# Kernel optimization log

Measured on AMD Instinct MI355X. Metric: run time of the kernel, lower is better.

Reference implementation:

```python
import jax, jax.numpy as jnp
import numpy as np

B, T, E, H = 4, 2048, 1024, 16
S = E // H  # 64


def setup_inputs() -> dict:
    key = jax.random.key(0)
    ks = jax.random.split(key, 6)
    return {
        "x": jax.random.normal(ks[0], (B, T, E), dtype=jnp.float32),
        "Wk": jax.random.normal(ks[1], (S, S), dtype=jnp.float32) * (1.0 / np.sqrt(S)),
        "Wq": jax.random.normal(ks[2], (S, S), dtype=jnp.float32) * (1.0 / np.sqrt(S)),
        "Wv": jax.random.normal(ks[3], (S, S), dtype=jnp.float32) * (1.0 / np.sqrt(S)),
        "Wp": jax.random.normal(ks[4], (E, E), dtype=jnp.float32) * (1.0 / np.sqrt(E)),
        "bp": jnp.zeros((E,), dtype=jnp.float32),
    }


def reference(x, Wk, Wq, Wv, Wp, bp):
    b, t, e = x.shape
    h, s = H, S
    xh = x.reshape(b, t, h, s)
    # per-head projections share one (s,s) weight across all heads (torch Linear: y = x @ W.T)
    keys = jnp.einsum('bthi,oi->bhto', xh, Wk)     # (b,h,t,s)
    queries = jnp.einsum('bthi,oi->bhto', xh, Wq)
    values = jnp.einsum('bthi,oi->bhto', xh, Wv)
    scale = e ** 0.25  # q and k each divided by e^(1/4) -> net 1/sqrt(e)
    queries = queries / scale
    keys = keys / scale
    dot = jnp.einsum('bhqs,bhks->bhqk', queries, keys)  # (b,h,t,t)
    attn = jax.nn.softmax(dot, axis=-1)
    out = jnp.einsum('bhqk,bhks->bqhs', attn, values)   # (b,t,h,s)
    out = out.reshape(b, t, h * s)
    return jnp.einsum('bte,oe->bto', out, Wp) + bp
```

## Files before the change

kernel.cpp:

```cpp
#include <hip/hip_runtime.h>
#include <hip/hip_bf16.h>

#define Bv 4
#define Tv 2048
#define Ev 1024
#define Hv 16
#define Sv 64

typedef __attribute__((ext_vector_type(8))) short bf16x8;
typedef __attribute__((ext_vector_type(4))) short bf16x4;
typedef __attribute__((ext_vector_type(4))) float f32x4;
typedef __attribute__((ext_vector_type(16))) float f32x16;

__device__ __forceinline__ ushort f2bf(float f) {
    unsigned u = __float_as_uint(f);
    u = (u + 0x7FFFu + ((u >> 16) & 1u)) >> 16;
    return (ushort)u;
}
__device__ __forceinline__ unsigned pkrn(float a, float b) {
    __hip_bfloat162 t = __float22bfloat162_rn(make_float2(a, b));
    unsigned r; __builtin_memcpy(&r, &t, 4); return r;
}
__device__ __forceinline__ unsigned pktr(float a, float b) {
    return __builtin_amdgcn_perm(__float_as_uint(b), __float_as_uint(a), 0x07060302u);
}

__device__ __forceinline__ void async16(void* lds, const void* g) {
    __builtin_amdgcn_global_load_lds(
        (const __attribute__((address_space(1))) unsigned int*)g,
        (__attribute__((address_space(3))) unsigned int*)lds, 16, 0, 0);
}

__global__ __launch_bounds__(256) void cast_kernel(
    const float* __restrict__ Wp, const float* __restrict__ Wq,
    const float* __restrict__ Wk, const float* __restrict__ Wv,
    ushort* __restrict__ Wpb, ushort* __restrict__ Wqb,
    ushort* __restrict__ Wkb, ushort* __restrict__ Wvb)
{
    int blk = blockIdx.x;
    if (blk < 1024) {
        int i = (blk * 256 + threadIdx.x) * 4;
        float4 v = *(const float4*)(Wp + i);
        uint2 o = {pkrn(v.x, v.y), pkrn(v.z, v.w)};
        *(uint2*)(Wpb + i) = o;
    } else {
        int p = blk - 1024;
        const float* src = (p == 0) ? Wq : ((p == 1) ? Wk : Wv);
        ushort* dst      = (p == 0) ? Wqb : ((p == 1) ? Wkb : Wvb);
        const float scale = (p == 0) ? 0.03125f * 1.4426950408889634f : 1.0f;
        #pragma unroll
        for (int it = 0; it < 4; ++it) {
            int i = (it * 256 + threadIdx.x) * 4;
            float4 v = *(const float4*)(src + i);
            uint2 o = {pkrn(v.x * scale, v.y * scale), pkrn(v.z * scale, v.w * scale)};
            *(uint2*)(dst + i) = o;
        }
    }
}

__global__ __launch_bounds__(192) void qkv_kernel(
    const float* __restrict__ x,
    const ushort* __restrict__ Wqb, const ushort* __restrict__ Wkb,
    const ushort* __restrict__ Wvb,
    ushort* __restrict__ Q, ushort* __restrict__ K, ushort* __restrict__ Vt)
{
    const int tid  = threadIdx.x;
    const int wave = tid >> 6;
    const int lane = tid & 63;
    const int m    = lane & 15;
    const int quad = lane >> 4;

    const ushort* Wsel = (wave == 0) ? Wqb : ((wave == 1) ? Wkb : Wvb);
    bf16x8 wf[4][2];
    #pragma unroll
    for (int ot = 0; ot < 4; ++ot)
        #pragma unroll
        for (int ks = 0; ks < 2; ++ks)
            wf[ot][ks] = *(const bf16x8*)&Wsel[(ot * 16 + m) * 64 + ks * 32 + quad * 8];

    const int tt = blockIdx.x >> 2;
    const int hg = blockIdx.x & 3;
    const int g0 = tt * 16;
    const int gm = g0 + m;
    const int b  = g0 >> 11;
    const int t0 = g0 & 2047;

    #pragma unroll
    for (int hi = 0; hi < 4; ++hi) {
        const int h  = hg * 4 + hi;
        const int bh = b * Hv + h;

        bf16x8 xf[2];
        #pragma unroll
        for (int ks = 0; ks < 2; ++ks) {
            const float* src = x + (size_t)gm * Ev + h * Sv + ks * 32 + quad * 8;
            float4 v0 = *(const float4*)src;
            float4 v1 = *(const float4*)(src + 4);
            unsigned pk[4];
            pk[0] = pkrn(v0.x, v0.y); pk[1] = pkrn(v0.z, v0.w);
            pk[2] = pkrn(v1.x, v1.y); pk[3] = pkrn(v1.z, v1.w);
            xf[ks] = *(bf16x8*)pk;
        }

        f32x4 acc[4];
        #pragma unroll
        for (int ot = 0; ot < 4; ++ot) acc[ot] = (f32x4){0.f, 0.f, 0.f, 0.f};

        if (wave < 2) {
            #pragma unroll
            for (int ks = 0; ks < 2; ++ks)
                #pragma unroll
                for (int ot = 0; ot < 4; ++ot)
                    acc[ot] = __builtin_amdgcn_mfma_f32_16x16x32_bf16(
                        wf[ot][ks], xf[ks], acc[ot], 0, 0, 0);
            ushort* dst = ((wave == 0) ? Q : K)
                        + ((size_t)bh * Tv + t0 + m) * Sv + quad * 4;
            #pragma unroll
            for (int ot = 0; ot < 4; ++ot) {
                uint2 w = {pkrn(acc[ot][0], acc[ot][1]), pkrn(acc[ot][2], acc[ot][3])};
                *(uint2*)(dst + ot * 16) = w;
            }
        } else {
            #pragma unroll
            for (int ks = 0; ks < 2; ++ks)
                #pragma unroll
                for (int st = 0; st < 4; ++st)
                    acc[st] = __builtin_amdgcn_mfma_f32_16x16x32_bf16(
                        xf[ks], wf[st][ks], acc[st], 0, 0, 0);
            ushort* vr = Vt + ((size_t)bh * Sv + m) * Tv + t0 + quad * 4;
            #pragma unroll
            for (int st = 0; st < 4; ++st) {
                uint2 w = {pkrn(acc[st][0], acc[st][1]), pkrn(acc[st][2], acc[st][3])};
                *(uint2*)(vr + (size_t)st * 16 * Tv) = w;
            }
        }
    }
}

__global__ __launch_bounds__(256, 4) void attn_kernel(
    const ushort* __restrict__ Q, const ushort* __restrict__ K,
    const ushort* __restrict__ Vt, ushort* __restrict__ O)
{
    __shared__ ushort kl[64 * 64];
    __shared__ ushort vl[64 * 64];
    __shared__ float  ll[4][32];

    const int tid  = threadIdx.x;
    const int wave = tid >> 6;
    const int lane = tid & 63;
    const int r31  = lane & 31;
    const int hi   = lane >> 5;
    const int bh   = blockIdx.x & 63;
    const int q0   = (blockIdx.x >> 6) << 7;

    const ushort* Qb = Q + ((size_t)bh * Tv + q0 + wave * 32 + r31) * Sv + hi * 8;
    bf16x8 qf[4];
    #pragma unroll
    for (int ks = 0; ks < 4; ++ks)
        qf[ks] = *(const bf16x8*)(Qb + ks * 16);

    f32x16 oa[2];
    #pragma unroll
    for (int st = 0; st < 2; ++st)
        #pragma unroll
        for (int r = 0; r < 16; ++r)
            oa[st][r] = 0.f;
    float lsum = 0.f;

    const ushort* Kb = K  + (size_t)bh * Tv * Sv;
    const ushort* Vb = Vt + (size_t)bh * Sv * Tv;

    const int r0 = tid >> 3,         cg0 = (tid & 7) ^ (r0 & 7);
    const int r1 = (256 + tid) >> 3, cg1 = ((256 + tid) & 7) ^ (r1 & 7);
    const size_t koff0 = (size_t)r0 * Sv + cg0 * 8;
    const size_t koff1 = (size_t)r1 * Sv + cg1 * 8;
    const size_t voff0 = (size_t)r0 * Tv + cg0 * 8;
    const size_t voff1 = (size_t)r1 * Tv + cg1 * 8;
    const int swz = r31 & 7;

    for (int k0 = 0; k0 < Tv; k0 += 64) {
        __syncthreads();
        async16(&kl[(size_t)tid * 8],         Kb + (size_t)k0 * Sv + koff0);
        async16(&kl[((size_t)tid + 256) * 8], Kb + (size_t)k0 * Sv + koff1);
        async16(&vl[(size_t)tid * 8],         Vb + k0 + voff0);
        async16(&vl[((size_t)tid + 256) * 8], Vb + k0 + voff1);
        __syncthreads();

        #pragma unroll
        for (int kt = 0; kt < 2; ++kt) {
            f32x16 sacc;
            #pragma unroll
            for (int r = 0; r < 16; ++r) sacc[r] = 0.f;
            #pragma unroll
            for (int ks = 0; ks < 4; ++ks) {
                bf16x8 kf = *(const bf16x8*)
                    &kl[(kt * 32 + r31) * 64 + (((ks * 2 + hi) ^ swz) * 8)];
                sacc = __builtin_amdgcn_mfma_f32_32x32x16_bf16(
                    kf, qf[ks], sacc, 0, 0, 0);
            }

            #pragma unroll
            for (int kp = 0; kp < 2; ++kp) {
                float p[8];
                #pragma unroll
                for (int j = 0; j < 8; ++j)
                    p[j] = __builtin_amdgcn_exp2f(sacc[kp * 8 + j]);
                lsum += ((p[0] + p[1]) + (p[2] + p[3]))
                      + ((p[4] + p[5]) + (p[6] + p[7]));
                unsigned d0 = pktr(p[0], p[1]);
                unsigned d1 = pktr(p[2], p[3]);
                unsigned d2 = pktr(p[4], p[5]);
                unsigned d3 = pktr(p[6], p[7]);
                asm volatile("v_permlane32_swap_b32 %0, %1"
                             : "+v"(d0), "+v"(d2));
                asm volatile("v_permlane32_swap_b32 %0, %1"
                             : "+v"(d1), "+v"(d3));
                unsigned pw[4] = {d0, d1, d2, d3};
                bf16x8 pf = *(bf16x8*)pw;

                const int kc = (kt * 2 + kp) * 2 + hi;
                #pragma unroll
                for (int st = 0; st < 2; ++st) {
                    bf16x8 vf = *(const bf16x8*)
                        &vl[(st * 32 + r31) * 64 + ((kc ^ swz) * 8)];
                    oa[st] = __builtin_amdgcn_mfma_f32_32x32x16_bf16(
                        pf, vf, oa[st], 0, 0, 0);
                }
            }
        }
    }

    lsum += __shfl_xor(lsum, 32, 64);
    if (lane < 32) ll[wave][lane] = 1.0f / lsum;

    float sc[16];
    #pragma unroll
    for (int r = 0; r < 16; ++r)
        sc[r] = ll[wave][(r & 3) + 4 * hi + 8 * (r >> 2)];

    const int b = bh >> 4, h = bh & 15;
    #pragma unroll
    for (int st = 0; st < 2; ++st)
        #pragma unroll
        for (int r = 0; r < 16; ++r) {
            const int q = (r & 3) + 4 * hi + 8 * (r >> 2);
            O[((size_t)(b * Tv + q0 + wave * 32 + q)) * Ev
              + h * Sv + st * 32 + r31] = f2bf(oa[st][r] * sc[r]);
        }
}

__global__ __launch_bounds__(256) void proj_kernel(
    const ushort* __restrict__ A, const ushort* __restrict__ B,
    const float* __restrict__ bp, float* __restrict__ C)
{
    __shared__ ushort Asm[128 * 32];
    __shared__ ushort Bsm[128 * 32];
    const int tid  = threadIdx.x;
    const int wave = tid >> 6;
    const int lane = tid & 63;
    const int m    = lane & 15;
    const int quad = lane >> 4;
    const int wm   = wave >> 1;
    const int wn   = wave & 1;
    const int m0   = blockIdx.x * 128;
    const int n0   = blockIdx.y * 128;

    f32x4 acc[4][4];
    #pragma unroll
    for (int i = 0; i < 4; ++i)
        #pragma unroll
        for (int j = 0; j < 4; ++j)
            acc[i][j] = (f32x4){0.f, 0.f, 0.f, 0.f};

    for (int k0 = 0; k0 < Ev; k0 += 32) {
        __syncthreads();
        #pragma unroll
        for (int j = 0; j < 2; ++j) {
            int c   = j * 256 + tid;
            int row = c >> 2;
            int col = (c & 3) * 8;
            async16(&Asm[c * 8], &A[(size_t)(m0 + row) * Ev + k0 + col]);
            async16(&Bsm[c * 8], &B[(size_t)(n0 + row) * Ev + k0 + col]);
        }
        __syncthreads();

        bf16x8 af[4], bf[4];
        #pragma unroll
        for (int i = 0; i < 4; ++i)
            af[i] = *(const bf16x8*)&Asm[(wm * 64 + i * 16 + m) * 32 + quad * 8];
        #pragma unroll
        for (int j = 0; j < 4; ++j)
            bf[j] = *(const bf16x8*)&Bsm[(wn * 64 + j * 16 + m) * 32 + quad * 8];
        #pragma unroll
        for (int i = 0; i < 4; ++i)
            #pragma unroll
            for (int j = 0; j < 4; ++j)
                acc[i][j] = __builtin_amdgcn_mfma_f32_16x16x32_bf16(
                    af[i], bf[j], acc[i][j], 0, 0, 0);
    }

    float bbv[4];
    #pragma unroll
    for (int j = 0; j < 4; ++j)
        bbv[j] = bp[n0 + wn * 64 + j * 16 + m];

    #pragma unroll
    for (int i = 0; i < 4; ++i)
        #pragma unroll
        for (int j = 0; j < 4; ++j)
            #pragma unroll
            for (int r = 0; r < 4; ++r)
                C[(size_t)(m0 + wm * 64 + i * 16 + quad * 4 + r) * Ev
                  + n0 + wn * 64 + j * 16 + m] = acc[i][j][r] + bbv[j];
}

extern "C" void kernel_launch(void* const* d_in, const int* in_sizes, int n_in,
                              void* d_out, int out_size, void* d_ws, size_t ws_size,
                              hipStream_t stream) {
    const float* x  = (const float*)d_in[0];
    const float* Wk = (const float*)d_in[1];
    const float* Wq = (const float*)d_in[2];
    const float* Wv = (const float*)d_in[3];
    const float* Wp = (const float*)d_in[4];
    const float* bp = (const float*)d_in[5];
    float* out = (float*)d_out;

    ushort* Q   = (ushort*)d_ws;
    ushort* K   = Q   + 8388608;
    ushort* Vt  = K   + 8388608;
    ushort* O   = Vt  + 8388608;
    ushort* Wpb = O   + 8388608;
    ushort* Wqb = Wpb + 1048576;
    ushort* Wkb = Wqb + 4096;
    ushort* Wvb = Wkb + 4096;

    cast_kernel<<<1027, 256, 0, stream>>>(Wp, Wq, Wk, Wv, Wpb, Wqb, Wkb, Wvb);
    qkv_kernel<<<2048, 192, 0, stream>>>(x, Wqb, Wkb, Wvb, Q, K, Vt);
    attn_kernel<<<1024, 256, 0, stream>>>(Q, K, Vt, O);
    proj_kernel<<<dim3(64, 8), 256, 0, stream>>>(O, Wpb, bp, out);
}
```

Measured before the change: 222.2 us.

## Process two 32-query groups per wave in attention to reuse K/V fragments

```diff
diff --git a/kernel.cpp b/kernel.cpp
--- a/kernel.cpp
+++ b/kernel.cpp
@@ -137,13 +137,13 @@
     }
 }
 
-__global__ __launch_bounds__(256, 4) void attn_kernel(
+__global__ __launch_bounds__(256, 2) void attn_kernel(
     const ushort* __restrict__ Q, const ushort* __restrict__ K,
     const ushort* __restrict__ Vt, ushort* __restrict__ O)
 {
     __shared__ ushort kl[64 * 64];
     __shared__ ushort vl[64 * 64];
-    __shared__ float  ll[4][32];
+    __shared__ float  ll[4][64];
 
     const int tid  = threadIdx.x;
     const int wave = tid >> 6;
@@ -151,21 +151,25 @@
     const int r31  = lane & 31;
     const int hi   = lane >> 5;
     const int bh   = blockIdx.x & 63;
-    const int q0   = (blockIdx.x >> 6) << 7;
-
-    const ushort* Qb = Q + ((size_t)bh * Tv + q0 + wave * 32 + r31) * Sv + hi * 8;
-    bf16x8 qf[4];
-    #pragma unroll
-    for (int ks = 0; ks < 4; ++ks)
-        qf[ks] = *(const bf16x8*)(Qb + ks * 16);
-
-    f32x16 oa[2];
-    #pragma unroll
-    for (int st = 0; st < 2; ++st)
-        #pragma unroll
-        for (int r = 0; r < 16; ++r)
-            oa[st][r] = 0.f;
-    float lsum = 0.f;
+    const int q0   = (blockIdx.x >> 6) << 8;
+
+    const ushort* Qb = Q + ((size_t)bh * Tv + q0 + wave * 64 + r31) * Sv + hi * 8;
+    bf16x8 qf[2][4];
+    #pragma unroll
+    for (int g = 0; g < 2; ++g)
+        #pragma unroll
+        for (int ks = 0; ks < 4; ++ks)
+            qf[g][ks] = *(const bf16x8*)(Qb + (size_t)g * 32 * Sv + ks * 16);
+
+    f32x16 oa[2][2];
+    #pragma unroll
+    for (int g = 0; g < 2; ++g)
+        #pragma unroll
+        for (int st = 0; st < 2; ++st)
+            #pragma unroll
+            for (int r = 0; r < 16; ++r)
+                oa[g][st][r] = 0.f;
+    float lsum[2] = {0.f, 0.f};
 
     const ushort* Kb = K  + (size_t)bh * Tv * Sv;
     const ushort* Vb = Vt + (size_t)bh * Sv * Tv;
@@ -178,6 +182,28 @@
     const size_t voff1 = (size_t)r1 * Tv + cg1 * 8;
     const int swz = r31 & 7;
 
+    auto softpv = [&](const f32x16& sv, float& ls, f32x16* oag, int kp,
+                      const bf16x8* vf) {
+        float p[8];
+        #pragma unroll
+        for (int j = 0; j < 8; ++j)
+            p[j] = __builtin_amdgcn_exp2f(sv[kp * 8 + j]);
+        ls += ((p[0] + p[1]) + (p[2] + p[3]))
+            + ((p[4] + p[5]) + (p[6] + p[7]));
+        unsigned d0 = pktr(p[0], p[1]);
+        unsigned d1 = pktr(p[2], p[3]);
+        unsigned d2 = pktr(p[4], p[5]);
+        unsigned d3 = pktr(p[6], p[7]);
+        asm volatile("v_permlane32_swap_b32 %0, %1" : "+v"(d0), "+v"(d2));
+        asm volatile("v_permlane32_swap_b32 %0, %1" : "+v"(d1), "+v"(d3));
+        unsigned pw[4] = {d0, d1, d2, d3};
+        bf16x8 pf = *(bf16x8*)pw;
+        #pragma unroll
+        for (int st = 0; st < 2; ++st)
+            oag[st] = __builtin_amdgcn_mfma_f32_32x32x16_bf16(
+                pf, vf[st], oag[st], 0, 0, 0);
+    };
+
     for (int k0 = 0; k0 < Tv; k0 += 64) {
         __syncthreads();
         async16(&kl[(size_t)tid * 8],         Kb + (size_t)k0 * Sv + koff0);
@@ -188,65 +214,61 @@
 
         #pragma unroll
         for (int kt = 0; kt < 2; ++kt) {
-            f32x16 sacc;
-            #pragma unroll
-            for (int r = 0; r < 16; ++r) sacc[r] = 0.f;
-            #pragma unroll
-            for (int ks = 0; ks < 4; ++ks) {
-                bf16x8 kf = *(const bf16x8*)
+            bf16x8 kf[4];
+            #pragma unroll
+            for (int ks = 0; ks < 4; ++ks)
+                kf[ks] = *(const bf16x8*)
                     &kl[(kt * 32 + r31) * 64 + (((ks * 2 + hi) ^ swz) * 8)];
-                sacc = __builtin_amdgcn_mfma_f32_32x32x16_bf16(
-                    kf, qf[ks], sacc, 0, 0, 0);
+
+            f32x16 s0, s1;
+            #pragma unroll
+            for (int r = 0; r < 16; ++r) { s0[r] = 0.f; s1[r] = 0.f; }
+            #pragma unroll
+            for (int ks = 0; ks < 4; ++ks)
+                s0 = __builtin_amdgcn_mfma_f32_32x32x16_bf16(
+                    kf[ks], qf[0][ks], s0, 0, 0, 0);
+            #pragma unroll
+            for (int ks = 0; ks < 4; ++ks)
+                s1 = __builtin_amdgcn_mfma_f32_32x32x16_bf16(
+                    kf[ks], qf[1][ks], s1, 0, 0, 0);
+
+            #pragma unroll
+            for (int kp = 0; kp < 2; ++kp) {
+                const int kc = (kt * 2 + kp) * 2 + hi;
+                bf16x8 vf[2];
+                #pragma unroll
+                for (int st = 0; st < 2; ++st)
+                    vf[st] = *(const bf16x8*)
+                        &vl[(st * 32 + r31) * 64 + ((kc ^ swz) * 8)];
+                softpv(s0, lsum[0], oa[0], kp, vf);
+                softpv(s1, lsum[1], oa[1], kp, vf);
             }
-
-            #pragma unroll
-            for (int kp = 0; kp < 2; ++kp) {
-                float p[8];
-                #pragma unroll
-                for (int j = 0; j < 8; ++j)
-                    p[j] = __builtin_amdgcn_exp2f(sacc[kp * 8 + j]);
-                lsum += ((p[0] + p[1]) + (p[2] + p[3]))
-                      + ((p[4] + p[5]) + (p[6] + p[7]));
-                unsigned d0 = pktr(p[0], p[1]);
-                unsigned d1 = pktr(p[2], p[3]);
-                unsigned d2 = pktr(p[4], p[5]);
-                unsigned d3 = pktr(p[6], p[7]);
-                asm volatile("v_permlane32_swap_b32 %0, %1"
-                             : "+v"(d0), "+v"(d2));
-                asm volatile("v_permlane32_swap_b32 %0, %1"
-                             : "+v"(d1), "+v"(d3));
-                unsigned pw[4] = {d0, d1, d2, d3};
-                bf16x8 pf = *(bf16x8*)pw;
-
-                const int kc = (kt * 2 + kp) * 2 + hi;
-                #pragma unroll
-                for (int st = 0; st < 2; ++st) {
-                    bf16x8 vf = *(const bf16x8*)
-                        &vl[(st * 32 + r31) * 64 + ((kc ^ swz) * 8)];
-                    oa[st] = __builtin_amdgcn_mfma_f32_32x32x16_bf16(
-                        pf, vf, oa[st], 0, 0, 0);
-                }
+        }
+    }
+
+    lsum[0] += __shfl_xor(lsum[0], 32, 64);
+    lsum[1] += __shfl_xor(lsum[1], 32, 64);
+    if (hi == 0) {
+        ll[wave][r31]      = 1.0f / lsum[0];
+        ll[wave][32 + r31] = 1.0f / lsum[1];
+    }
+
+    const int b = bh >> 4, h = bh & 15;
+    #pragma unroll
+    for (int g = 0; g < 2; ++g) {
+        float sc[16];
+        #pragma unroll
+        for (int r = 0; r < 16; ++r)
+            sc[r] = ll[wave][g * 32 + (r & 3) + 4 * hi + 8 * (r >> 2)];
+        #pragma unroll
+        for (int st = 0; st < 2; ++st)
+            #pragma unroll
+            for (int r = 0; r < 16; ++r) {
+                const int q = (r & 3) + 4 * hi + 8 * (r >> 2);
+                O[((size_t)(b * Tv + q0 + wave * 64 + g * 32 + q)) * Ev
+                  + h * Sv + st * 32 + r31] = f2bf(oa[g][st][r] * sc[r]);
             }
-        }
-    }
-
-    lsum += __shfl_xor(lsum, 32, 64);
-    if (lane < 32) ll[wave][lane] = 1.0f / lsum;
-
-    float sc[16];
-    #pragma unroll
-    for (int r = 0; r < 16; ++r)
-        sc[r] = ll[wave][(r & 3) + 4 * hi + 8 * (r >> 2)];
-
-    const int b = bh >> 4, h = bh & 15;
-    #pragma unroll
-    for (int st = 0; st < 2; ++st)
-        #pragma unroll
-        for (int r = 0; r < 16; ++r) {
-            const int q = (r & 3) + 4 * hi + 8 * (r >> 2);
-            O[((size_t)(b * Tv + q0 + wave * 32 + q)) * Ev
-              + h * Sv + st * 32 + r31] = f2bf(oa[st][r] * sc[r]);
-        }
+    }
 }
 
 __global__ __launch_bounds__(256) void proj_kernel(
@@ -336,6 +358,6 @@
 
     cast_kernel<<<1027, 256, 0, stream>>>(Wp, Wq, Wk, Wv, Wpb, Wqb, Wkb, Wvb);
     qkv_kernel<<<2048, 192, 0, stream>>>(x, Wqb, Wkb, Wvb, Q, K, Vt);
-    attn_kernel<<<1024, 256, 0, stream>>>(Q, K, Vt, O);
+    attn_kernel<<<512, 256, 0, stream>>>(Q, K, Vt, O);
     proj_kernel<<<dim3(64, 8), 256, 0, stream>>>(O, Wpb, bp, out);
 }
```

New measurement: 218.2 us. Within noise of the previous version (-1.8%).
